# Kernel tuning notes

Measured on AMD Instinct MI355X. Metric: run time of the kernel, lower is better.

Reference implementation:

```python
import jax, jax.numpy as jnp
import numpy as np

B, N, K, F_IN, F_OUT = 8, 2048, 32, 256, 256


def setup_inputs() -> dict:
    key = jax.random.key(0)
    ks = jax.random.split(key, 8)
    x = jax.random.normal(ks[0], (B, N, F_IN), dtype=jnp.float32)
    idx_neib = jax.random.randint(ks[1], (N, K), 0, N, dtype=jnp.int32)
    # Linear params (torch nn.Linear stores weight as [out, in])
    lim_x = np.sqrt(2.0) * np.sqrt(6.0 / (F_IN + F_OUT))  # xavier_uniform, gain=relu
    Wx_w = jax.random.uniform(ks[2], (F_OUT, F_IN), jnp.float32, -lim_x, lim_x)
    Wx_b = jnp.zeros((F_OUT,), jnp.float32)
    Wn_w = jax.random.uniform(ks[3], (F_OUT, F_IN), jnp.float32, -lim_x, lim_x)
    Wn_b = jnp.zeros((F_OUT,), jnp.float32)
    gamma = jnp.ones((2 * F_OUT,), jnp.float32)
    beta = jnp.zeros((2 * F_OUT,), jnp.float32)
    return {"x": x, "idx_neib": idx_neib, "Wx_w": Wx_w, "Wx_b": Wx_b,
            "Wn_w": Wn_w, "Wn_b": Wn_b, "gamma": gamma, "beta": beta}


def reference(x, idx_neib, Wx_w, Wx_b, Wn_w, Wn_b, gamma, beta):
    # Gather neighbor features: [B, N, K, F] then mean over the K neighbors.
    x_neib = jnp.take(x, idx_neib, axis=1).mean(axis=2)  # [B, N, F]
    # Dual linear projections (weights stored [out, in] as in torch).
    h_self = jnp.einsum('bnf,of->bno', x, Wx_w) + Wx_b
    h_nei = jnp.einsum('bnf,of->bno', x_neib, Wn_w) + Wn_b
    h = jnp.concatenate([h_self, h_nei], axis=2)          # [B, N, 2*out]
    # F.normalize(p=2, dim=2): divide by max(||h||_2, 1e-12)
    nrm = jnp.sqrt(jnp.sum(h * h, axis=2, keepdims=True))
    h = h / jnp.maximum(nrm, 1e-12)
    h = jax.nn.relu(h)
    # BatchNorm1d over channel dim (training mode: batch stats over B and N,
    # biased variance), eps=1e-5.
    mu = h.mean(axis=(0, 1))
    var = jnp.mean((h - mu) ** 2, axis=(0, 1))
    h = (h - mu) * jax.lax.rsqrt(var + 1e-5) * gamma + beta
    return h
```

## Files before the change

kernel.cpp:

```cpp
#include <hip/hip_runtime.h>
#include <stdint.h>

#define BB 8
#define NN 2048
#define KK 32
#define FIN 256
#define FOUT 256
#define CC 512
#define MM (BB*NN)
#define RB 32
#define NBLK (MM/RB)
#define LDA 264

typedef __attribute__((ext_vector_type(8))) short short8;
typedef __attribute__((ext_vector_type(4))) float f32x4;

__device__ __forceinline__ unsigned short f2bf(float f) {
    union { float f; unsigned u; } v; v.f = f;
    unsigned u = v.u;
    return (unsigned short)((u + 0x7FFFu + ((u >> 16) & 1u)) >> 16);
}
__device__ __forceinline__ float bf2f(unsigned short s) {
    union { unsigned u; float f; } v; v.u = ((unsigned)s) << 16;
    return v.f;
}

__global__ void k_prep(const float* __restrict__ Wx, const float* __restrict__ Wxb,
                       const float* __restrict__ Wn, const float* __restrict__ Wnb,
                       const float* __restrict__ x,
                       unsigned short* __restrict__ Wc, float* __restrict__ bc,
                       unsigned short* __restrict__ xb) {
    const int blk = blockIdx.x;
    const int tid = threadIdx.x;
    if (blk < 128) {
        int gid = blk * 256 + tid;
        int e0 = gid * 4;
        int o = e0 >> 8, k = e0 & 255;
        const float* src = (o < FOUT) ? (Wx + o * FIN + k) : (Wn + (o - FOUT) * FIN + k);
        float4 v = *(const float4*)src;
        ushort4 p; p.x = f2bf(v.x); p.y = f2bf(v.y); p.z = f2bf(v.z); p.w = f2bf(v.w);
        *(ushort4*)(Wc + e0) = p;
        if (gid < 128) {
            int c0 = gid * 4;
            float4 bv = (c0 < FOUT) ? *(const float4*)(Wxb + c0)
                                    : *(const float4*)(Wnb + c0 - FOUT);
            *(float4*)(bc + c0) = bv;
        }
    } else {
        size_t gid = (size_t)(blk - 128) * 256 + tid;
        size_t e0 = gid * 8;
        float4 v0 = *(const float4*)(x + e0);
        float4 v1 = *(const float4*)(x + e0 + 4);
        ushort4 p0, p1;
        p0.x = f2bf(v0.x); p0.y = f2bf(v0.y); p0.z = f2bf(v0.z); p0.w = f2bf(v0.w);
        p1.x = f2bf(v1.x); p1.y = f2bf(v1.y); p1.z = f2bf(v1.z); p1.w = f2bf(v1.w);
        *(ushort4*)(xb + e0)     = p0;
        *(ushort4*)(xb + e0 + 4) = p1;
    }
}

__global__ __launch_bounds__(256, 2)
void k_gemm(const unsigned short* __restrict__ xb, const int* __restrict__ idx,
            const unsigned short* __restrict__ Wc,
            const float* __restrict__ bc,
            unsigned short* __restrict__ h,
            float* __restrict__ psum, float* __restrict__ psq) {
    __shared__ unsigned short As[2][RB * LDA];
    __shared__ float sqpart[4][RB];
    __shared__ float rnorm[RB];

    const int bid  = blockIdx.x;
    const int tid  = threadIdx.x;
    const int w    = tid >> 6;
    const int lane = tid & 63;
    const int quad = lane >> 4;
    const int l16  = lane & 15;
    const int b    = bid & 7;
    const int n0   = (bid >> 3) * RB;
    const unsigned short* xbat = xb + (size_t)b * NN * FIN;
    const size_t r0g = (size_t)b * NN + n0;

    {
        const uint4* gs = (const uint4*)(xbat + (size_t)n0 * FIN);
        #pragma unroll
        for (int i = 0; i < 4; ++i) {
            int e = tid + i * 256;
            *(uint4*)&As[0][(e >> 5) * LDA + (e & 31) * 8] = gs[e];
        }
    }
    {
        #pragma unroll
        for (int rr = 0; rr < 8; ++rr) {
            int lr = w * 8 + rr;
            const int* ip = idx + (n0 + lr) * KK;
            const unsigned short* xp = xbat + lane * 4;
            float a0 = 0.f, a1 = 0.f, a2 = 0.f, a3 = 0.f;
            #pragma unroll 8
            for (int k = 0; k < KK; ++k) {
                ushort4 v = *(const ushort4*)(xp + (size_t)ip[k] * FIN);
                a0 += bf2f(v.x); a1 += bf2f(v.y); a2 += bf2f(v.z); a3 += bf2f(v.w);
            }
            const float s = 1.0f / (float)KK;
            ushort4 o4; o4.x = f2bf(a0 * s); o4.y = f2bf(a1 * s);
            o4.z = f2bf(a2 * s); o4.w = f2bf(a3 * s);
            *(ushort4*)&As[1][lr * LDA + lane * 4] = o4;
        }
    }
    __syncthreads();

    const unsigned short* A = As[w >> 1];
    const int cb = w * 128;

    f32x4 acc[2][8];
    #pragma unroll
    for (int mt = 0; mt < 2; ++mt)
        #pragma unroll
        for (int nt = 0; nt < 8; ++nt) acc[mt][nt] = (f32x4){0.f, 0.f, 0.f, 0.f};

    const unsigned short* Bp = Wc + (size_t)(cb + l16) * FIN + quad * 8;
    const unsigned short* Ap = A + (size_t)l16 * LDA + quad * 8;

    #pragma unroll 2
    for (int k0 = 0; k0 < FIN; k0 += 32) {
        short8 a0 = *(const short8*)(Ap + k0);
        short8 a1 = *(const short8*)(Ap + 16 * LDA + k0);
        short8 bfr[8];
        #pragma unroll
        for (int nt = 0; nt < 8; ++nt)
            bfr[nt] = *(const short8*)(Bp + (size_t)nt * 16 * FIN + k0);
        #pragma unroll
        for (int nt = 0; nt < 8; ++nt) {
            acc[0][nt] = __builtin_amdgcn_mfma_f32_16x16x32_bf16(a0, bfr[nt], acc[0][nt], 0, 0, 0);
            acc[1][nt] = __builtin_amdgcn_mfma_f32_16x16x32_bf16(a1, bfr[nt], acc[1][nt], 0, 0, 0);
        }
    }

    float bcv[8];
    #pragma unroll
    for (int nt = 0; nt < 8; ++nt) bcv[nt] = bc[cb + nt * 16 + l16];

    float rsq[2][4] = {{0.f,0.f,0.f,0.f},{0.f,0.f,0.f,0.f}};
    #pragma unroll
    for (int mt = 0; mt < 2; ++mt)
        #pragma unroll
        for (int nt = 0; nt < 8; ++nt)
            #pragma unroll
            for (int r = 0; r < 4; ++r) {
                float v = acc[mt][nt][r] + bcv[nt];
                acc[mt][nt][r] = v;
                rsq[mt][r] += v * v;
            }
    #pragma unroll
    for (int off = 1; off < 16; off <<= 1)
        #pragma unroll
        for (int mt = 0; mt < 2; ++mt)
            #pragma unroll
            for (int r = 0; r < 4; ++r)
                rsq[mt][r] += __shfl_xor(rsq[mt][r], off, 64);
    if (l16 == 0) {
        #pragma unroll
        for (int mt = 0; mt < 2; ++mt)
            #pragma unroll
            for (int r = 0; r < 4; ++r)
                sqpart[w][mt * 16 + quad * 4 + r] = rsq[mt][r];
    }
    __syncthreads();
    if (tid < RB) {
        float tot = sqpart[0][tid] + sqpart[1][tid] + sqpart[2][tid] + sqpart[3][tid];
        rnorm[tid] = 1.0f / fmaxf(sqrtf(tot), 1e-12f);
    }
    __syncthreads();

    float csum[8] = {0.f,0.f,0.f,0.f,0.f,0.f,0.f,0.f};
    float csq [8] = {0.f,0.f,0.f,0.f,0.f,0.f,0.f,0.f};
    #pragma unroll
    for (int mt = 0; mt < 2; ++mt) {
        #pragma unroll
        for (int r = 0; r < 4; ++r) {
            int row = mt * 16 + quad * 4 + r;
            float rn = rnorm[row];
            unsigned short* hp = h + (r0g + row) * CC + cb + l16;
            #pragma unroll
            for (int nt = 0; nt < 8; ++nt) {
                float v = fmaxf(acc[mt][nt][r] * rn, 0.0f);
                hp[nt * 16] = f2bf(v);
                csum[nt] += v;
                csq [nt] += v * v;
            }
        }
    }
    #pragma unroll
    for (int off = 16; off < 64; off <<= 1)
        #pragma unroll
        for (int nt = 0; nt < 8; ++nt) {
            csum[nt] += __shfl_xor(csum[nt], off, 64);
            csq [nt] += __shfl_xor(csq [nt], off, 64);
        }
    if (quad == 0) {
        #pragma unroll
        for (int nt = 0; nt < 8; ++nt) {
            int c = cb + nt * 16 + l16;
            psum[(size_t)c * NBLK + bid] = csum[nt];
            psq [(size_t)c * NBLK + bid] = csq [nt];
        }
    }
}

__global__ void k_stats(const float* __restrict__ psum, const float* __restrict__ psq,
                        const float* __restrict__ gamma, const float* __restrict__ beta,
                        float* __restrict__ ss) {
    __shared__ float ps[4], pq[4];
    int c = blockIdx.x, t = threadIdx.x;
    float s = psum[(size_t)c * NBLK + t] + psum[(size_t)c * NBLK + 256 + t];
    float q = psq [(size_t)c * NBLK + t] + psq [(size_t)c * NBLK + 256 + t];
    #pragma unroll
    for (int off = 32; off; off >>= 1) { s += __shfl_xor(s, off, 64); q += __shfl_xor(q, off, 64); }
    int w = t >> 6, lane = t & 63;
    if (lane == 0) { ps[w] = s; pq[w] = q; }
    __syncthreads();
    if (t == 0) {
        float S = ps[0] + ps[1] + ps[2] + ps[3];
        float Q = pq[0] + pq[1] + pq[2] + pq[3];
        const float inv = 1.0f / (float)MM;
        float mu  = S * inv;
        float var = fmaxf(Q * inv - mu * mu, 0.0f);
        float sc  = gamma[c] * rsqrtf(var + 1e-5f);
        ss[c]      = sc;
        ss[CC + c] = beta[c] - mu * sc;
    }
}

__global__ void k_apply(const unsigned short* __restrict__ h,
                        const float* __restrict__ ss,
                        float* __restrict__ out) {
    int gid = blockIdx.x * 256 + threadIdx.x;
    int c0 = (gid * 8) & (CC - 1);
    uint4 hv = ((const uint4*)h)[gid];
    const unsigned short* hs = (const unsigned short*)&hv;
    float4 sc0 = *(const float4*)(ss + c0);
    float4 sc1 = *(const float4*)(ss + c0 + 4);
    float4 sh0 = *(const float4*)(ss + CC + c0);
    float4 sh1 = *(const float4*)(ss + CC + c0 + 4);
    float4 o0, o1;
    o0.x = bf2f(hs[0]) * sc0.x + sh0.x;
    o0.y = bf2f(hs[1]) * sc0.y + sh0.y;
    o0.z = bf2f(hs[2]) * sc0.z + sh0.z;
    o0.w = bf2f(hs[3]) * sc0.w + sh0.w;
    o1.x = bf2f(hs[4]) * sc1.x + sh1.x;
    o1.y = bf2f(hs[5]) * sc1.y + sh1.y;
    o1.z = bf2f(hs[6]) * sc1.z + sh1.z;
    o1.w = bf2f(hs[7]) * sc1.w + sh1.w;
    ((float4*)out)[gid * 2]     = o0;
    ((float4*)out)[gid * 2 + 1] = o1;
}

extern "C" void kernel_launch(void* const* d_in, const int* in_sizes, int n_in,
                              void* d_out, int out_size, void* d_ws, size_t ws_size,
                              hipStream_t stream) {
    const float* x     = (const float*)d_in[0];
    const int*   idx   = (const int*)  d_in[1];
    const float* Wx_w  = (const float*)d_in[2];
    const float* Wx_b  = (const float*)d_in[3];
    const float* Wn_w  = (const float*)d_in[4];
    const float* Wn_b  = (const float*)d_in[5];
    const float* gamma = (const float*)d_in[6];
    const float* beta  = (const float*)d_in[7];
    float* out = (float*)d_out;

    char* p = (char*)d_ws;
    unsigned short* xb = (unsigned short*)p; p += (size_t)MM * FIN * 2;
    unsigned short* Wc = (unsigned short*)p; p += (size_t)CC * FIN * 2;
    float* bc          = (float*)p;          p += (size_t)CC * 4;
    unsigned short* h  = (unsigned short*)p; p += (size_t)MM * CC * 2;
    float* psum        = (float*)p;          p += (size_t)CC * NBLK * 4;
    float* psq         = (float*)p;          p += (size_t)CC * NBLK * 4;
    float* ss          = (float*)p;          p += (size_t)2 * CC * 4;

    hipLaunchKernelGGL(k_prep,  dim3(2176), dim3(256), 0, stream,
                       Wx_w, Wx_b, Wn_w, Wn_b, x, Wc, bc, xb);
    hipLaunchKernelGGL(k_gemm,  dim3(NBLK), dim3(256), 0, stream, xb, idx, Wc, bc, h, psum, psq);
    hipLaunchKernelGGL(k_stats, dim3(CC),   dim3(256), 0, stream, psum, psq, gamma, beta, ss);
    hipLaunchKernelGGL(k_apply, dim3(4096), dim3(256), 0, stream, h, ss, out);
}
```

Before: 141.7 us.

## Double k_gemm block to 512 threads with 16-byte split-K neighbor gather

The fused gather+GEMM kernel now runs 8 waves per block instead of 4. Each wave produces 64 output columns instead of 128, halving accumulator registers per thread. The neighbor-mean gather now loads 16-byte vectors, with the two half-waves each summing half of the K neighbors and combining through a cross-lane shuffle. The goal is more latency hiding for the random gathers and MFMA work, at the cost of more shuffles and a larger block-level reduction for the row norms.

```diff
diff --git a/kernel.cpp b/kernel.cpp
--- a/kernel.cpp
+++ b/kernel.cpp
@@ -59,14 +59,14 @@
     }
 }
 
-__global__ __launch_bounds__(256, 2)
+__global__ __launch_bounds__(512, 4)
 void k_gemm(const unsigned short* __restrict__ xb, const int* __restrict__ idx,
             const unsigned short* __restrict__ Wc,
             const float* __restrict__ bc,
             unsigned short* __restrict__ h,
             float* __restrict__ psum, float* __restrict__ psq) {
     __shared__ unsigned short As[2][RB * LDA];
-    __shared__ float sqpart[4][RB];
+    __shared__ float sqpart[8][RB];
     __shared__ float rnorm[RB];
 
     const int bid  = blockIdx.x;
@@ -75,6 +75,8 @@
     const int lane = tid & 63;
     const int quad = lane >> 4;
     const int l16  = lane & 15;
+    const int p    = lane >> 5;
+    const int l32  = lane & 31;
     const int b    = bid & 7;
     const int n0   = (bid >> 3) * RB;
     const unsigned short* xbat = xb + (size_t)b * NN * FIN;
@@ -83,67 +85,76 @@
     {
         const uint4* gs = (const uint4*)(xbat + (size_t)n0 * FIN);
         #pragma unroll
-        for (int i = 0; i < 4; ++i) {
-            int e = tid + i * 256;
+        for (int i = 0; i < 2; ++i) {
+            int e = tid + i * 512;
             *(uint4*)&As[0][(e >> 5) * LDA + (e & 31) * 8] = gs[e];
         }
     }
     {
         #pragma unroll
-        for (int rr = 0; rr < 8; ++rr) {
-            int lr = w * 8 + rr;
+        for (int rr = 0; rr < 4; ++rr) {
+            int lr = (w << 2) + rr;
             const int* ip = idx + (n0 + lr) * KK;
-            const unsigned short* xp = xbat + lane * 4;
-            float a0 = 0.f, a1 = 0.f, a2 = 0.f, a3 = 0.f;
+            const unsigned short* xp = xbat + l32 * 8;
+            float ac[8] = {0.f,0.f,0.f,0.f,0.f,0.f,0.f,0.f};
             #pragma unroll 8
-            for (int k = 0; k < KK; ++k) {
-                ushort4 v = *(const ushort4*)(xp + (size_t)ip[k] * FIN);
-                a0 += bf2f(v.x); a1 += bf2f(v.y); a2 += bf2f(v.z); a3 += bf2f(v.w);
-            }
-            const float s = 1.0f / (float)KK;
-            ushort4 o4; o4.x = f2bf(a0 * s); o4.y = f2bf(a1 * s);
-            o4.z = f2bf(a2 * s); o4.w = f2bf(a3 * s);
-            *(ushort4*)&As[1][lr * LDA + lane * 4] = o4;
-        }
-    }
-    __syncthreads();
-
-    const unsigned short* A = As[w >> 1];
-    const int cb = w * 128;
-
-    f32x4 acc[2][8];
+            for (int k = 0; k < 16; ++k) {
+                int j = ip[(k << 1) | p];
+                uint4 v = *(const uint4*)(xp + (size_t)j * FIN);
+                const unsigned short* hv = (const unsigned short*)&v;
+                #pragma unroll
+                for (int c = 0; c < 8; ++c) ac[c] += bf2f(hv[c]);
+            }
+            #pragma unroll
+            for (int c = 0; c < 8; ++c) ac[c] += __shfl_xor(ac[c], 32, 64);
+            if (p == 0) {
+                const float s = 1.0f / (float)KK;
+                unsigned short o8[8];
+                #pragma unroll
+                for (int c = 0; c < 8; ++c) o8[c] = f2bf(ac[c] * s);
+                *(uint4*)&As[1][lr * LDA + l32 * 8] = *(const uint4*)o8;
+            }
+        }
+    }
+    __syncthreads();
+
+    const int half = w >> 2;
+    const unsigned short* A = As[half];
+    const int cbg = half * 256 + (w & 3) * 64;
+
+    f32x4 acc[2][4];
     #pragma unroll
     for (int mt = 0; mt < 2; ++mt)
         #pragma unroll
-        for (int nt = 0; nt < 8; ++nt) acc[mt][nt] = (f32x4){0.f, 0.f, 0.f, 0.f};
-
-    const unsigned short* Bp = Wc + (size_t)(cb + l16) * FIN + quad * 8;
+        for (int nt = 0; nt < 4; ++nt) acc[mt][nt] = (f32x4){0.f, 0.f, 0.f, 0.f};
+
+    const unsigned short* Bp = Wc + (size_t)(cbg + l16) * FIN + quad * 8;
     const unsigned short* Ap = A + (size_t)l16 * LDA + quad * 8;
 
     #pragma unroll 2
     for (int k0 = 0; k0 < FIN; k0 += 32) {
         short8 a0 = *(const short8*)(Ap + k0);
         short8 a1 = *(const short8*)(Ap + 16 * LDA + k0);
-        short8 bfr[8];
-        #pragma unroll
-        for (int nt = 0; nt < 8; ++nt)
+        short8 bfr[4];
+        #pragma unroll
+        for (int nt = 0; nt < 4; ++nt)
             bfr[nt] = *(const short8*)(Bp + (size_t)nt * 16 * FIN + k0);
         #pragma unroll
-        for (int nt = 0; nt < 8; ++nt) {
+        for (int nt = 0; nt < 4; ++nt) {
             acc[0][nt] = __builtin_amdgcn_mfma_f32_16x16x32_bf16(a0, bfr[nt], acc[0][nt], 0, 0, 0);
             acc[1][nt] = __builtin_amdgcn_mfma_f32_16x16x32_bf16(a1, bfr[nt], acc[1][nt], 0, 0, 0);
         }
     }
 
-    float bcv[8];
-    #pragma unroll
-    for (int nt = 0; nt < 8; ++nt) bcv[nt] = bc[cb + nt * 16 + l16];
+    float bcv[4];
+    #pragma unroll
+    for (int nt = 0; nt < 4; ++nt) bcv[nt] = bc[cbg + nt * 16 + l16];
 
     float rsq[2][4] = {{0.f,0.f,0.f,0.f},{0.f,0.f,0.f,0.f}};
     #pragma unroll
     for (int mt = 0; mt < 2; ++mt)
         #pragma unroll
-        for (int nt = 0; nt < 8; ++nt)
+        for (int nt = 0; nt < 4; ++nt)
             #pragma unroll
             for (int r = 0; r < 4; ++r) {
                 float v = acc[mt][nt][r] + bcv[nt];
@@ -166,22 +177,24 @@
     }
     __syncthreads();
     if (tid < RB) {
-        float tot = sqpart[0][tid] + sqpart[1][tid] + sqpart[2][tid] + sqpart[3][tid];
+        float tot = 0.f;
+        #pragma unroll
+        for (int i = 0; i < 8; ++i) tot += sqpart[i][tid];
         rnorm[tid] = 1.0f / fmaxf(sqrtf(tot), 1e-12f);
     }
     __syncthreads();
 
-    float csum[8] = {0.f,0.f,0.f,0.f,0.f,0.f,0.f,0.f};
-    float csq [8] = {0.f,0.f,0.f,0.f,0.f,0.f,0.f,0.f};
+    float csum[4] = {0.f,0.f,0.f,0.f};
+    float csq [4] = {0.f,0.f,0.f,0.f};
     #pragma unroll
     for (int mt = 0; mt < 2; ++mt) {
         #pragma unroll
         for (int r = 0; r < 4; ++r) {
             int row = mt * 16 + quad * 4 + r;
             float rn = rnorm[row];
-            unsigned short* hp = h + (r0g + row) * CC + cb + l16;
-            #pragma unroll
-            for (int nt = 0; nt < 8; ++nt) {
+            unsigned short* hp = h + (r0g + row) * CC + cbg + l16;
+            #pragma unroll
+            for (int nt = 0; nt < 4; ++nt) {
                 float v = fmaxf(acc[mt][nt][r] * rn, 0.0f);
                 hp[nt * 16] = f2bf(v);
                 csum[nt] += v;
@@ -192,14 +205,14 @@
     #pragma unroll
     for (int off = 16; off < 64; off <<= 1)
         #pragma unroll
-        for (int nt = 0; nt < 8; ++nt) {
+        for (int nt = 0; nt < 4; ++nt) {
             csum[nt] += __shfl_xor(csum[nt], off, 64);
             csq [nt] += __shfl_xor(csq [nt], off, 64);
         }
     if (quad == 0) {
         #pragma unroll
-        for (int nt = 0; nt < 8; ++nt) {
-            int c = cb + nt * 16 + l16;
+        for (int nt = 0; nt < 4; ++nt) {
+            int c = cbg + nt * 16 + l16;
             psum[(size_t)c * NBLK + bid] = csum[nt];
             psq [(size_t)c * NBLK + bid] = csq [nt];
         }
@@ -278,7 +291,7 @@
 
     hipLaunchKernelGGL(k_prep,  dim3(2176), dim3(256), 0, stream,
                        Wx_w, Wx_b, Wn_w, Wn_b, x, Wc, bc, xb);
-    hipLaunchKernelGGL(k_gemm,  dim3(NBLK), dim3(256), 0, stream, xb, idx, Wc, bc, h, psum, psq);
+    hipLaunchKernelGGL(k_gemm,  dim3(NBLK), dim3(512), 0, stream, xb, idx, Wc, bc, h, psum, psq);
     hipLaunchKernelGGL(k_stats, dim3(CC),   dim3(256), 0, stream, psum, psq, gamma, beta, ss);
     hipLaunchKernelGGL(k_apply, dim3(4096), dim3(256), 0, stream, h, ss, out);
 }
```

Result: faster. 130.4 us (-8.0%).
